# Performance work log

Measured on AMD Instinct MI355X. Metric: run time of the kernel, lower is better.

The kernel has to match this reference:

```python
import jax, jax.numpy as jnp
import numpy as np

PERIOD = 15          # hardcoded in the torch module's forward: STL(series, 15)
N_SEASONAL = 7       # statsmodels STL default seasonal smoother length
N_TREND = 29         # smallest odd >= 1.5*p/(1-1.5/7) = 28.64 -> 29 (statsmodels default)
N_LOWPASS = 17       # smallest odd > period (statsmodels default)
N_INNER = 2          # statsmodels: robust=False -> 2 inner iterations, 0 outer


def _loess_matrix(n, q, ts):
    """Dense linear operator for degree-1 LOESS smoothing of a length-n series
    evaluated at (possibly out-of-range) integer positions ts. Non-robust LOESS is
    linear in y, so smoothing == matmul with this constant matrix."""
    M = np.zeros((len(ts), n), dtype=np.float64)
    qq = min(q, n)
    for i, t in enumerate(ts):
        left = int(np.clip(t - (q - 1) // 2, 0, n - qq))
        right = left + qq - 1
        h = max(t - left, right - t)
        if q > n:
            h += (q - n) / 2.0
        xs = np.arange(left, right + 1, dtype=np.float64)
        w = np.clip(1.0 - (np.abs(xs - t) / h) ** 3, 0.0, None) ** 3  # tricube
        w = w / w.sum()
        xbar = (w * xs).sum()
        var = (w * (xs - xbar) ** 2).sum()
        a = w.copy()
        if var > 1e-12:  # degree-1 local linear fit; fall back to deg-0 if degenerate
            a = w * (1.0 + (t - xbar) * (xs - xbar) / var)
        M[i, left:right + 1] = a
    return M.astype(np.float32)


def _ma(x, k):
    """Moving average of window k along last axis (valid mode)."""
    cs = jnp.cumsum(x, axis=-1)
    cs = jnp.concatenate([jnp.zeros(x.shape[:-1] + (1,), x.dtype), cs], axis=-1)
    return (cs[..., k:] - cs[..., :-k]) / k


def setup_inputs() -> dict:
    key = jax.random.key(0)
    x = jax.random.normal(key, (128, 480, 256), dtype=jnp.float32)  # [B, T, C]
    return {"x": x}


def reference(x):
    B, T, Cc = x.shape
    p = PERIOD
    n_sub = T // p  # cycle-subseries length; T chosen divisible by period

    # Constant LOESS smoothing operators (numpy, baked in as jit constants)
    M_seas = jnp.asarray(_loess_matrix(n_sub, N_SEASONAL, np.arange(-1, n_sub + 1)))  # (n_sub+2, n_sub)
    M_lp = jnp.asarray(_loess_matrix(T, N_LOWPASS, np.arange(T)))                     # (T, T)
    M_trend = jnp.asarray(_loess_matrix(T, N_TREND, np.arange(T)))                    # (T, T)

    y = jnp.transpose(x, (0, 2, 1))  # [B, C, T]
    trend = jnp.zeros_like(y)
    seasonal = jnp.zeros_like(y)

    for _ in range(N_INNER):  # STL inner loop (Cleveland 1990, non-robust)
        # 1. detrend
        D = y - trend
        # 2. cycle-subseries LOESS smoothing, extended one period each side
        Dsub = D.reshape(B, Cc, n_sub, p)                      # subseries along axis 2
        Cext = jnp.einsum('sn,bcnp->bcsp', M_seas, Dsub)       # [B,C,n_sub+2,p]
        Cext = Cext.reshape(B, Cc, (n_sub + 2) * p)            # time order, length T+2p
        # 3. low-pass: MA(p) x2, MA(3), then LOESS(n_l)
        lp = _ma(_ma(_ma(Cext, p), p), 3)                      # length T
        L = jnp.einsum('tn,bcn->bct', M_lp, lp)
        # 4. seasonal = smoothed subseries (center T) minus low-pass
        seasonal = Cext[..., p:p + T] - L
        # 5+6. deseasonalize and trend LOESS
        trend = jnp.einsum('tn,bcn->bct', M_trend, y - seasonal)

    resid = y - seasonal - trend
    seas_plus_resid = jnp.transpose(seasonal + resid, (0, 2, 1))  # [B, T, C]
    trend_out = jnp.transpose(trend, (0, 2, 1))
    return (seas_plus_resid, trend_out)
```

## Files before the change

kernel.cpp:

```cpp
#include <hip/hip_runtime.h>
#include <hip/hip_bf16.h>
#include <stdint.h>

#define TLEN 480
#define NB 128
#define NC 256

typedef short bf16x8 __attribute__((ext_vector_type(8)));
typedef float f32x4 __attribute__((ext_vector_type(4)));
typedef unsigned short u16;
typedef unsigned int u32;

__device__ inline u16 f2bf(float f) {
    union { float f; uint32_t u; } v; v.f = f;
    uint32_t u = v.u;
    return (u16)((u + 0x7fffu + ((u >> 16) & 1u)) >> 16);
}

__device__ inline u32 pack2bf(float lo, float hi) {
    return __builtin_amdgcn_perm(__float_as_uint(hi), __float_as_uint(lo), 0x07060302u);
}

template<int N, int Q>
__device__ __forceinline__ int loess_wT(int t, float* out) {
    int left = t - (Q - 1) / 2;
    if (left < 0) left = 0;
    if (left > N - Q) left = N - Q;
    int right = left + Q - 1;
    int h = (t - left) > (right - t) ? (t - left) : (right - t);
    double w[Q];
    double wsum = 0.0;
    #pragma unroll
    for (int i = 0; i < Q; ++i) {
        double dist = fabs((double)(left + i - t)) / (double)h;
        double u = 1.0 - dist * dist * dist;
        if (u < 0.0) u = 0.0;
        double wv = u * u * u;
        w[i] = wv; wsum += wv;
    }
    #pragma unroll
    for (int i = 0; i < Q; ++i) w[i] /= wsum;
    double xbar = 0.0;
    #pragma unroll
    for (int i = 0; i < Q; ++i) xbar += w[i] * (double)(left + i);
    double var = 0.0;
    #pragma unroll
    for (int i = 0; i < Q; ++i) { double d = (double)(left + i) - xbar; var += w[i] * d * d; }
    if (var > 1e-12) {
        double tb = (double)t - xbar;
        #pragma unroll
        for (int i = 0; i < Q; ++i) {
            double d = (double)(left + i) - xbar;
            out[i] = (float)(w[i] * (1.0 + tb * d / var));
        }
    } else {
        #pragma unroll
        for (int i = 0; i < Q; ++i) out[i] = (float)w[i];
    }
    return left;
}

__global__ void k_loess(float* Ms, float* w3, float* MlpC, float* MtC) {
    int gid = blockIdx.x * 256 + threadIdx.x;
    if (gid < 34) {
        float wl[7];
        int left = loess_wT<32, 7>(gid - 1, wl);
        float* row = Ms + gid * 32;
        #pragma unroll
        for (int i = 0; i < 32; ++i) row[i] = 0.0f;
        #pragma unroll
        for (int i = 0; i < 7; ++i) row[left + i] = wl[i];
    } else if (gid < 514) {
        int t = gid - 34;
        float wl[17];
        loess_wT<TLEN, 17>(t, wl);
        #pragma unroll
        for (int i = 0; i < 17; ++i) MlpC[t * 17 + i] = wl[i];
    } else if (gid < 994) {
        int t = gid - 514;
        float wl[29];
        loess_wT<TLEN, 29>(t, wl);
        #pragma unroll
        for (int i = 0; i < 29; ++i) MtC[t * 29 + i] = wl[i];
    } else if (gid < 1025) {
        int d = gid - 994;
        int cnt = 0;
        for (int c = 0; c < 3; ++c)
            for (int a = 0; a < 15; ++a) {
                int b = d - a - c;
                if (b >= 0 && b < 15) cnt++;
            }
        w3[d] = (float)((double)cnt / 675.0);
    }
}

__global__ void k_S(const float* __restrict__ Ms, const float* __restrict__ w3,
                    const float* __restrict__ MlpC, float* __restrict__ S) {
    int id = blockIdx.x * 256 + threadIdx.x;
    if (id >= TLEN * TLEN) return;
    int t = id / TLEN, u = id - t * TLEN;
    int nu = u / 15, ju = u - nu * 15;
    int slp = t - 8;
    if (slp < 0) slp = 0;
    if (slp > TLEN - 17) slp = TLEN - 17;
    float acc = 0.0f;
    for (int k = 0; k < 17; ++k) {
        int i = slp + k;
        int s_lo = (i - ju + 14) / 15;
        float g = 0.0f;
        #pragma unroll
        for (int ds = 0; ds < 3; ++ds) {
            int s = s_lo + ds;
            int d = s * 15 + ju - i;
            if (s >= 0 && s < 34 && d >= 0 && d <= 30)
                g += Ms[s * 32 + nu] * w3[d];
        }
        acc += MlpC[t * 17 + k] * g;
    }
    float val = -acc;
    if (t % 15 == ju) val += Ms[(1 + t / 15) * 32 + nu];
    S[id] = val;
}

__global__ void k_VU(const float* __restrict__ MtC, const float* __restrict__ S,
                     float* __restrict__ U, float* __restrict__ V) {
    int id = blockIdx.x * 256 + threadIdx.x;
    if (id >= TLEN * TLEN) return;
    int t = id / TLEN, u = id - t * TLEN;
    int st = t - 14;
    if (st < 0) st = 0;
    if (st > TLEN - 29) st = TLEN - 29;
    float acc = 0.0f;
    for (int k = 0; k < 29; ++k)
        acc += MtC[t * 29 + k] * S[(size_t)(st + k) * TLEN + u];
    float mt = (u >= st && u < st + 29) ? MtC[t * 29 + (u - st)] : 0.0f;
    V[id] = acc;
    U[id] = mt - acc;
}

__global__ void k_A(const float* __restrict__ U, const float* __restrict__ V,
                    u16* __restrict__ Abf) {
    __shared__ float Vs[16][17];
    __shared__ float Us[16][17];
    int tx = threadIdx.x, ty = threadIdx.y;
    int u = blockIdx.x * 16 + tx;
    int t = blockIdx.y * 16 + ty;
    float acc = 0.0f;
    for (int kt = 0; kt < 30; ++kt) {
        Vs[ty][tx] = V[(size_t)t * TLEN + kt * 16 + tx];
        Us[ty][tx] = U[(size_t)(kt * 16 + ty) * TLEN + u];
        __syncthreads();
        #pragma unroll
        for (int e = 0; e < 16; ++e) acc += Vs[ty][e] * Us[e][tx];
        __syncthreads();
    }
    Abf[(size_t)t * TLEN + u] = f2bf(U[(size_t)t * TLEN + u] + acc);
}

__global__ __launch_bounds__(256, 4)
void k_gemm(const u16* __restrict__ A, const float* __restrict__ x,
            float* __restrict__ out0, float* __restrict__ out1) {
    __shared__ u16 Xs[32 * 488];
    int b = blockIdx.x;
    int t0 = blockIdx.y * 96;
    int cz = blockIdx.z * 32;
    int tid = threadIdx.x;
    int wave = tid >> 6, lane = tid & 63;
    int lane15 = lane & 15, quad = lane >> 4;
    int wt = wave & 1, wc = wave >> 1;

    int cq  = tid & 7;
    int kq0 = tid >> 3;
    const float* xp0 = x + (size_t)b * TLEN * NC + (size_t)(kq0 * 4) * NC + cz + cq * 4;
    u32* l32 = (u32*)Xs;
    int lbase = (cq * 4) * 244 + kq0 * 2;

    float4 r[16];
    #pragma unroll
    for (int p = 0; p < 4; ++p) {
        if (p < 3 || kq0 < 24) {
            const float* xp = xp0 + (size_t)p * 128 * NC;
            #pragma unroll
            for (int q = 0; q < 4; ++q) r[p * 4 + q] = *(const float4*)(xp + q * NC);
        }
    }
    #pragma unroll
    for (int p = 0; p < 4; ++p) {
        if (p < 3 || kq0 < 24) {
            const float* fl = (const float*)&r[p * 4];
            int o = lbase + p * 64;
            #pragma unroll
            for (int cc = 0; cc < 4; ++cc) {
                uint2 w;
                w.x = pack2bf(fl[0 * 4 + cc], fl[1 * 4 + cc]);
                w.y = pack2bf(fl[2 * 4 + cc], fl[3 * 4 + cc]);
                *(uint2*)(l32 + o + cc * 244) = w;
            }
        }
    }
    __syncthreads();

    const u16* bp0 = A + (size_t)(t0 + wt * 48 + lane15) * TLEN + quad * 8;
    int arow = (wc * 16 + lane15) * 488 + quad * 8;

    f32x4 acc[3] = {};
    bf16x8 B[3][3];
    bf16x8 Af[2];
    #pragma unroll
    for (int j = 0; j < 3; ++j) {
        B[0][j] = *(const bf16x8*)(bp0 + (size_t)j * 16 * TLEN);
        B[1][j] = *(const bf16x8*)(bp0 + (size_t)j * 16 * TLEN + 32);
    }
    Af[0] = *(const bf16x8*)&Xs[arow];

    #pragma unroll
    for (int s = 0; s < 15; ++s) {
        const int cs = s % 3;
        const int ns = (s + 2) % 3;
        const int pa = s & 1, na = (s & 1) ^ 1;
        if (s < 13) {
            int k = (s + 2) * 32;
            #pragma unroll
            for (int j = 0; j < 3; ++j)
                B[ns][j] = *(const bf16x8*)(bp0 + (size_t)j * 16 * TLEN + k);
        }
        if (s < 14)
            Af[na] = *(const bf16x8*)&Xs[arow + (s + 1) * 32];
        #pragma unroll
        for (int j = 0; j < 3; ++j)
            acc[j] = __builtin_amdgcn_mfma_f32_16x16x32_bf16(Af[pa], B[cs][j], acc[j], 0, 0, 0);
    }

    __syncthreads();

    float* T = (float*)Xs;
    float* R = T + 96 * 36;
    #pragma unroll
    for (int j = 0; j < 3; ++j) {
        int tl = wt * 48 + j * 16 + lane15;
        int clb = wc * 16 + quad * 4;
        f32x4 tv = acc[j];
        size_t gb = ((size_t)b * TLEN + t0 + tl) * NC + cz + clb;
        f32x4 xv = *(const f32x4*)(x + gb);
        *(f32x4*)&T[tl * 36 + clb] = tv;
        *(f32x4*)&R[tl * 36 + clb] = xv - tv;
    }
    __syncthreads();

    #pragma unroll
    for (int v = 0; v < 3; ++v) {
        int id = v * 256 + tid;
        int tl = id >> 3, c4 = (id & 7) * 4;
        size_t gb = ((size_t)b * TLEN + t0 + tl) * NC + cz + c4;
        f32x4 tv = *(const f32x4*)&T[tl * 36 + c4];
        f32x4 rv = *(const f32x4*)&R[tl * 36 + c4];
        __builtin_nontemporal_store(tv, (f32x4*)(out1 + gb));
        __builtin_nontemporal_store(rv, (f32x4*)(out0 + gb));
    }
}

extern "C" void kernel_launch(void* const* d_in, const int* in_sizes, int n_in,
                              void* d_out, int out_size, void* d_ws, size_t ws_size,
                              hipStream_t stream) {
    const float* x = (const float*)d_in[0];
    float* out0 = (float*)d_out;
    float* out1 = (float*)d_out + (size_t)NB * TLEN * NC;

    char* ws = (char*)d_ws;
    size_t oMs  = 0;
    size_t oW3  = oMs + 4352;
    size_t oLpC = oW3 + 128;
    size_t oMtC = oLpC + 32640;
    size_t oS   = oMtC + 55680;
    size_t oU   = oS + 921600;
    size_t oV   = oU + 921600;
    size_t oA   = oV + 921600;

    float* Ms   = (float*)(ws + oMs);
    float* w3   = (float*)(ws + oW3);
    float* MlpC = (float*)(ws + oLpC);
    float* MtC  = (float*)(ws + oMtC);
    float* S    = (float*)(ws + oS);
    float* U    = (float*)(ws + oU);
    float* V    = (float*)(ws + oV);
    u16*   Abf  = (u16*)(ws + oA);

    k_loess<<<5, 256, 0, stream>>>(Ms, w3, MlpC, MtC);
    k_S<<<900, 256, 0, stream>>>(Ms, w3, MlpC, S);
    k_VU<<<900, 256, 0, stream>>>(MtC, S, U, V);
    k_A<<<dim3(30, 30), dim3(16, 16), 0, stream>>>(U, V, Abf);
    k_gemm<<<dim3(NB, 5, 8), 256, 0, stream>>>(Abf, x, out0, out1);
}
```

Baseline: 281.0 us.

## Pipeline k-loop in GEMM with double-buffered LDS and async A loads

```diff
diff --git a/kernel.cpp b/kernel.cpp
--- a/kernel.cpp
+++ b/kernel.cpp
@@ -19,6 +19,13 @@
 
 __device__ inline u32 pack2bf(float lo, float hi) {
     return __builtin_amdgcn_perm(__float_as_uint(hi), __float_as_uint(lo), 0x07060302u);
+}
+
+__device__ __forceinline__ void glds16(const void* g, void* l) {
+    __builtin_amdgcn_global_load_lds(
+        (const __attribute__((address_space(1))) unsigned int*)g,
+        (__attribute__((address_space(3))) unsigned int*)l,
+        16, 0, 0);
 }
 
 template<int N, int Q>
@@ -160,102 +167,90 @@
 __global__ __launch_bounds__(256, 4)
 void k_gemm(const u16* __restrict__ A, const float* __restrict__ x,
             float* __restrict__ out0, float* __restrict__ out1) {
-    __shared__ u16 Xs[32 * 488];
+    __shared__ __align__(16) char lds_raw[26112];
+    u16* xbuf = (u16*)lds_raw;
+    u16* abuf = (u16*)(lds_raw + 10240);
+
     int b = blockIdx.x;
     int t0 = blockIdx.y * 96;
-    int cz = blockIdx.z * 32;
+    int cz = blockIdx.z * 64;
     int tid = threadIdx.x;
     int wave = tid >> 6, lane = tid & 63;
     int lane15 = lane & 15, quad = lane >> 4;
-    int wt = wave & 1, wc = wave >> 1;
-
-    int cq  = tid & 7;
-    int kq0 = tid >> 3;
-    const float* xp0 = x + (size_t)b * TLEN * NC + (size_t)(kq0 * 4) * NC + cz + cq * 4;
-    u32* l32 = (u32*)Xs;
-    int lbase = (cq * 4) * 244 + kq0 * 2;
-
-    float4 r[16];
-    #pragma unroll
-    for (int p = 0; p < 4; ++p) {
-        if (p < 3 || kq0 < 24) {
-            const float* xp = xp0 + (size_t)p * 128 * NC;
-            #pragma unroll
-            for (int q = 0; q < 4; ++q) r[p * 4 + q] = *(const float4*)(xp + q * NC);
-        }
-    }
-    #pragma unroll
-    for (int p = 0; p < 4; ++p) {
-        if (p < 3 || kq0 < 24) {
-            const float* fl = (const float*)&r[p * 4];
-            int o = lbase + p * 64;
-            #pragma unroll
-            for (int cc = 0; cc < 4; ++cc) {
-                uint2 w;
-                w.x = pack2bf(fl[0 * 4 + cc], fl[1 * 4 + cc]);
-                w.y = pack2bf(fl[2 * 4 + cc], fl[3 * 4 + cc]);
-                *(uint2*)(l32 + o + cc * 244) = w;
-            }
-        }
-    }
+    int wc = wave & 1, wt = wave >> 1;
+
+    int kk2 = tid & 15;
+    int cq  = tid >> 4;
+    const float* xg = x + (size_t)b * TLEN * NC + cz + cq * 4;
+
+    int lrow = lane >> 2, lcol = lane & 3;
+    const u16* ag = A + (size_t)(t0 + lrow) * TLEN + lcol * 8;
+
+    float4 rs[2][2];
+
+    #define XLOAD(dst, s) { const float* p_ = xg + (size_t)((s) * 32 + 2 * kk2) * NC; \
+        dst[0] = *(const float4*)p_; dst[1] = *(const float4*)(p_ + NC); }
+    #define XPACK(src, h) { u32* o_ = (u32*)(xbuf + (h) * 2560); int bo_ = cq * 80 + kk2; \
+        o_[bo_]      = pack2bf(src[0].x, src[1].x); \
+        o_[bo_ + 20] = pack2bf(src[0].y, src[1].y); \
+        o_[bo_ + 40] = pack2bf(src[0].z, src[1].z); \
+        o_[bo_ + 60] = pack2bf(src[0].w, src[1].w); }
+    #define ASTAGE(s, h) { \
+        glds16(ag + (size_t)(wave * 16) * TLEN + (s) * 32, abuf + (h) * 3072 + wave * 512); \
+        if (wave < 2) \
+            glds16(ag + (size_t)((wave + 4) * 16) * TLEN + (s) * 32, abuf + (h) * 3072 + (wave + 4) * 512); }
+
+    XLOAD(rs[0], 0);
+    ASTAGE(0, 0);
+    XLOAD(rs[1], 1);
+    XPACK(rs[0], 0);
     __syncthreads();
 
-    const u16* bp0 = A + (size_t)(t0 + wt * 48 + lane15) * TLEN + quad * 8;
-    int arow = (wc * 16 + lane15) * 488 + quad * 8;
-
-    f32x4 acc[3] = {};
-    bf16x8 B[3][3];
-    bf16x8 Af[2];
-    #pragma unroll
-    for (int j = 0; j < 3; ++j) {
-        B[0][j] = *(const bf16x8*)(bp0 + (size_t)j * 16 * TLEN);
-        B[1][j] = *(const bf16x8*)(bp0 + (size_t)j * 16 * TLEN + 32);
-    }
-    Af[0] = *(const bf16x8*)&Xs[arow];
-
+    f32x4 acc[2][3] = {};
     #pragma unroll
     for (int s = 0; s < 15; ++s) {
-        const int cs = s % 3;
-        const int ns = (s + 2) % 3;
-        const int pa = s & 1, na = (s & 1) ^ 1;
-        if (s < 13) {
-            int k = (s + 2) * 32;
-            #pragma unroll
-            for (int j = 0; j < 3; ++j)
-                B[ns][j] = *(const bf16x8*)(bp0 + (size_t)j * 16 * TLEN + k);
-        }
-        if (s < 14)
-            Af[na] = *(const bf16x8*)&Xs[arow + (s + 1) * 32];
-        #pragma unroll
-        for (int j = 0; j < 3; ++j)
-            acc[j] = __builtin_amdgcn_mfma_f32_16x16x32_bf16(Af[pa], B[cs][j], acc[j], 0, 0, 0);
-    }
-
+        const int cur = s & 1, nxt = cur ^ 1;
+        if (s < 14) {
+            ASTAGE(s + 1, nxt);
+            if (s < 13) XLOAD(rs[s & 1], s + 2);
+            XPACK(rs[(s + 1) & 1], nxt);
+        }
+        const u32* xb = (const u32*)xbuf + cur * 1280 + (wc * 32 + lane15) * 20 + quad * 4;
+        bf16x8 a0 = *(const bf16x8*)xb;
+        bf16x8 a1 = *(const bf16x8*)(xb + 320);
+        const u16* ab = abuf + cur * 3072 + (wt * 48 + lane15) * 32 + quad * 8;
+        #pragma unroll
+        for (int j = 0; j < 3; ++j) {
+            bf16x8 bb = *(const bf16x8*)(ab + j * 512);
+            acc[0][j] = __builtin_amdgcn_mfma_f32_16x16x32_bf16(a0, bb, acc[0][j], 0, 0, 0);
+            acc[1][j] = __builtin_amdgcn_mfma_f32_16x16x32_bf16(a1, bb, acc[1][j], 0, 0, 0);
+        }
+        __syncthreads();
+    }
+    #undef XLOAD
+    #undef XPACK
+    #undef ASTAGE
+
+    float* T = (float*)lds_raw;
+    #pragma unroll
+    for (int i = 0; i < 2; ++i)
+        #pragma unroll
+        for (int j = 0; j < 3; ++j) {
+            int tl = wt * 48 + j * 16 + lane15;
+            int cl = wc * 32 + i * 16 + quad * 4;
+            *(f32x4*)&T[tl * 68 + cl] = acc[i][j];
+        }
     __syncthreads();
 
-    float* T = (float*)Xs;
-    float* R = T + 96 * 36;
-    #pragma unroll
-    for (int j = 0; j < 3; ++j) {
-        int tl = wt * 48 + j * 16 + lane15;
-        int clb = wc * 16 + quad * 4;
-        f32x4 tv = acc[j];
-        size_t gb = ((size_t)b * TLEN + t0 + tl) * NC + cz + clb;
+    #pragma unroll
+    for (int v = 0; v < 6; ++v) {
+        int id = v * 256 + tid;
+        int tl = id >> 4, c4 = (id & 15) * 4;
+        size_t gb = ((size_t)b * TLEN + t0 + tl) * NC + cz + c4;
+        f32x4 tv = *(const f32x4*)&T[tl * 68 + c4];
         f32x4 xv = *(const f32x4*)(x + gb);
-        *(f32x4*)&T[tl * 36 + clb] = tv;
-        *(f32x4*)&R[tl * 36 + clb] = xv - tv;
-    }
-    __syncthreads();
-
-    #pragma unroll
-    for (int v = 0; v < 3; ++v) {
-        int id = v * 256 + tid;
-        int tl = id >> 3, c4 = (id & 7) * 4;
-        size_t gb = ((size_t)b * TLEN + t0 + tl) * NC + cz + c4;
-        f32x4 tv = *(const f32x4*)&T[tl * 36 + c4];
-        f32x4 rv = *(const f32x4*)&R[tl * 36 + c4];
         __builtin_nontemporal_store(tv, (f32x4*)(out1 + gb));
-        __builtin_nontemporal_store(rv, (f32x4*)(out0 + gb));
+        __builtin_nontemporal_store(xv - tv, (f32x4*)(out0 + gb));
     }
 }
 
@@ -289,5 +284,5 @@
     k_S<<<900, 256, 0, stream>>>(Ms, w3, MlpC, S);
     k_VU<<<900, 256, 0, stream>>>(MtC, S, U, V);
     k_A<<<dim3(30, 30), dim3(16, 16), 0, stream>>>(U, V, Abf);
-    k_gemm<<<dim3(NB, 5, 8), 256, 0, stream>>>(Abf, x, out0, out1);
-}
+    k_gemm<<<dim3(NB, 5, 4), 256, 0, stream>>>(Abf, x, out0, out1);
+}
```

Measured after the change: 271.7 us. 1.03x faster.
